# Kernel tuning notes

Measured on AMD Instinct MI355X. Metric: run time of the kernel, lower is better.

Reference implementation:

```python
import jax, jax.numpy as jnp
import numpy as np


def setup_inputs() -> dict:
    key = jax.random.key(0)
    k1, k2 = jax.random.split(key)
    B, Lq, Ls, D = 16, 2048, 2048, 512
    query = jax.random.normal(k1, (B, Lq, D), dtype=jnp.float32)
    support = jax.random.normal(k2, (B, Ls, D), dtype=jnp.float32)
    return {"query": query, "support": support}


def reference(query, support):
    # attn: [B, Lq, Ls] = softmax(query @ support^T, axis=-1)
    logits = jnp.einsum("bqd,bsd->bqs", query, support)
    attn = jax.nn.softmax(logits, axis=-1)
    # attended support: [B, Lq, D]
    attended = jnp.einsum("bqs,bsd->bqd", attn, support)
    # score: [B, Lq] = sum over D of query * attended
    score = jnp.sum(query * attended, axis=-1)
    return score
```

## Files before the change

### kernel.cpp

```cpp
#include <hip/hip_runtime.h>
#include <hip/hip_bf16.h>

#define B_  16
#define LQ  2048
#define LS  2048
#define DD  512
#define BQ  256
#define BS  256
#define BK  32
#define NSB (LS / BS)
#define NKC (DD / BK)
#define NSPLIT 2
#define T_STAGES ((NSB / NSPLIT) * NKC)

typedef short bf16x8 __attribute__((ext_vector_type(8)));
typedef float f32x4  __attribute__((ext_vector_type(4)));
typedef unsigned short u16x8 __attribute__((ext_vector_type(8)));

__device__ __forceinline__ void load_lds16(const void* g, void* l) {
  __builtin_amdgcn_global_load_lds((const __attribute__((address_space(1))) void*)g,
                                   (__attribute__((address_space(3))) void*)l,
                                   16, 0, 0);
}

__device__ __forceinline__ unsigned short f2bf(float f) {
  union { float f; unsigned int u; } v; v.f = f;
  unsigned int r = v.u + 0x7fffu + ((v.u >> 16) & 1u);
  return (unsigned short)(r >> 16);
}

__global__ __launch_bounds__(256) void cvt_kernel(const float* __restrict__ Q,
                                                  const float* __restrict__ S,
                                                  unsigned short* __restrict__ Qw,
                                                  unsigned short* __restrict__ Sw,
                                                  int nblk) {
  int blk = blockIdx.x;
  const float* src; unsigned short* dst;
  if (blk < nblk) { src = Q; dst = Qw; } else { src = S; dst = Sw; blk -= nblk; }
  int i = blk * 256 + threadIdx.x;
  float4 f0 = ((const float4*)src)[i * 2];
  float4 f1 = ((const float4*)src)[i * 2 + 1];
  u16x8 u;
  u[0] = f2bf(f0.x); u[1] = f2bf(f0.y); u[2] = f2bf(f0.z); u[3] = f2bf(f0.w);
  u[4] = f2bf(f1.x); u[5] = f2bf(f1.y); u[6] = f2bf(f1.z); u[7] = f2bf(f1.w);
  ((u16x8*)dst)[i] = u;
}

__global__ __launch_bounds__(1024, 4) void attn_kernel(const unsigned short* __restrict__ Qw,
                                                       const unsigned short* __restrict__ Sw,
                                                       float* __restrict__ pm,
                                                       float* __restrict__ pse,
                                                       float* __restrict__ psel) {
  __shared__ __align__(16) unsigned short sQ0[BQ * BK], sS0[BS * BK];
  __shared__ __align__(16) unsigned short sQ1[BQ * BK], sS1[BS * BK];
  __shared__ __align__(16) unsigned short sQ2[BQ * BK], sS2[BS * BK];
  __shared__ __align__(16) unsigned short sQ3[BQ * BK], sS3[BS * BK];

  const int id   = blockIdx.x;
  const int qb   = id >> 5;
  const int bsx  = id & 31;
  const int b    = bsx >> 1;
  const int spl  = bsx & 1;
  const int tid  = threadIdx.x;
  const int w    = tid >> 6;
  const int lane = tid & 63;
  const int h    = w & 3;
  const int g    = w >> 2;
  const int col  = lane & 15;
  const int quad = lane >> 4;

  const int q0 = qb * BQ;
  const unsigned short* Qb = Qw + (size_t)b * LQ * DD;
  const unsigned short* Sb = Sw + (size_t)b * LS * DD;

  float mst[4] = { -INFINITY, -INFINITY, -INFINITY, -INFINITY };
  float se[4]  = { 0.f, 0.f, 0.f, 0.f };
  float sel[4] = { 0.f, 0.f, 0.f, 0.f };
  f32x4 acc[4][4];

  const int qrow   = 16 * w + (lane >> 2);
  const int cchunk = (lane & 3) ^ ((lane >> 2) & 3) ^ ((lane >> 4) & 3);
  const int ldsoff = w * 512;

  const int sbs = spl * (NSB / NSPLIT);

  auto issue = [&](int t, unsigned short* bq, unsigned short* bss) {
    const int ts = t < T_STAGES ? t : T_STAGES - 1;
    const int kb = (ts & 15) * BK + cchunk * 8;
    const int s0 = (sbs + (ts >> 4)) * BS;
    load_lds16(Qb + (size_t)(q0 + qrow) * DD + kb, bq + ldsoff);
    load_lds16(Sb + (size_t)(s0 + qrow) * DD + kb, bss + ldsoff);
  };

  const int pos = (quad ^ (col & 3) ^ ((col >> 2) & 3)) * 8;

  auto compute = [&](const unsigned short* bq, const unsigned short* bss) {
    bf16x8 aq[4], asv[4];
#pragma unroll
    for (int qt = 0; qt < 4; ++qt)
      aq[qt] = *(const bf16x8*)&bq[(g * 64 + qt * 16 + col) * BK + pos];
#pragma unroll
    for (int st = 0; st < 4; ++st)
      asv[st] = *(const bf16x8*)&bss[(h * 64 + st * 16 + col) * BK + pos];
#pragma unroll
    for (int st = 0; st < 4; ++st)
#pragma unroll
      for (int qt = 0; qt < 4; ++qt)
        acc[st][qt] = __builtin_amdgcn_mfma_f32_16x16x32_bf16(asv[st], aq[qt], acc[st][qt], 0, 0, 0);
  };

  auto initacc = [&]() {
#pragma unroll
    for (int st = 0; st < 4; ++st)
#pragma unroll
      for (int qt = 0; qt < 4; ++qt)
        acc[st][qt] = (f32x4){0.f, 0.f, 0.f, 0.f};
  };

  auto epilogue = [&]() {
#pragma unroll
    for (int qt = 0; qt < 4; ++qt) {
      float lmax = mst[qt];
#pragma unroll
      for (int st = 0; st < 4; ++st)
#pragma unroll
        for (int r = 0; r < 4; ++r)
          lmax = fmaxf(lmax, acc[st][qt][r]);
      lmax = fmaxf(lmax, __shfl_xor(lmax, 16, 64));
      lmax = fmaxf(lmax, __shfl_xor(lmax, 32, 64));
      float alpha = __expf(mst[qt] - lmax);
      float pe = 0.f, pel = 0.f;
#pragma unroll
      for (int st = 0; st < 4; ++st)
#pragma unroll
        for (int r = 0; r < 4; ++r) {
          float l = acc[st][qt][r];
          float e = __expf(l - lmax);
          pe += e;
          pel = fmaf(e, l, pel);
        }
      pe  += __shfl_xor(pe, 16, 64);  pe  += __shfl_xor(pe, 32, 64);
      pel += __shfl_xor(pel, 16, 64); pel += __shfl_xor(pel, 32, 64);
      se[qt]  = fmaf(se[qt],  alpha, pe);
      sel[qt] = fmaf(sel[qt], alpha, pel);
      mst[qt] = lmax;
    }
  };

#define STEP(t, RQ, RS, WQ, WS)                                   \
  do {                                                            \
    asm volatile("s_waitcnt vmcnt(4)" ::: "memory");              \
    asm volatile("s_barrier" ::: "memory");                       \
    issue((t) + 3, WQ, WS);                                       \
    if (((t) & 15) == 0) initacc();                               \
    compute(RQ, RS);                                              \
    if (((t) & 15) == 15) epilogue();                             \
  } while (0)

  issue(0, sQ0, sS0);
  issue(1, sQ1, sS1);
  issue(2, sQ2, sS2);

  for (int tt = 0; tt < T_STAGES; tt += 4) {
    STEP(tt + 0, sQ0, sS0, sQ3, sS3);
    STEP(tt + 1, sQ1, sS1, sQ0, sS0);
    STEP(tt + 2, sQ2, sS2, sQ1, sS1);
    STEP(tt + 3, sQ3, sS3, sQ2, sS2);
  }
#undef STEP

  __syncthreads();
  float* red = (float*)&sQ0[0];
  if (quad == 0) {
#pragma unroll
    for (int qt = 0; qt < 4; ++qt) {
      int idx = ((g * 4 + h) * 4 + qt) * 16 + col;
      red[idx]        = mst[qt];
      red[1024 + idx] = se[qt];
      red[2048 + idx] = sel[qt];
    }
  }
  __syncthreads();
  if (h == 0 && quad == 0) {
#pragma unroll
    for (int qt = 0; qt < 4; ++qt) {
      float M = -INFINITY;
#pragma unroll
      for (int hh = 0; hh < 4; ++hh)
        M = fmaxf(M, red[((g * 4 + hh) * 4 + qt) * 16 + col]);
      float SE = 0.f, SEL = 0.f;
#pragma unroll
      for (int hh = 0; hh < 4; ++hh) {
        int idx = ((g * 4 + hh) * 4 + qt) * 16 + col;
        float a = __expf(red[idx] - M);
        SE  = fmaf(red[1024 + idx], a, SE);
        SEL = fmaf(red[2048 + idx], a, SEL);
      }
      size_t qi = (size_t)b * LQ + q0 + g * 64 + qt * 16 + col;
      pm[qi * NSPLIT + spl]   = M;
      pse[qi * NSPLIT + spl]  = SE;
      psel[qi * NSPLIT + spl] = SEL;
    }
  }
}

__global__ __launch_bounds__(256) void combine_kernel(const float* __restrict__ pm,
                                                      const float* __restrict__ pse,
                                                      const float* __restrict__ psel,
                                                      float* __restrict__ out) {
  int i = blockIdx.x * blockDim.x + threadIdx.x;
  if (i >= B_ * LQ) return;
  float M = -INFINITY;
#pragma unroll
  for (int s = 0; s < NSPLIT; ++s) M = fmaxf(M, pm[i * NSPLIT + s]);
  float SE = 0.f, SEL = 0.f;
#pragma unroll
  for (int s = 0; s < NSPLIT; ++s) {
    float a = __expf(pm[i * NSPLIT + s] - M);
    SE  = fmaf(pse[i * NSPLIT + s],  a, SE);
    SEL = fmaf(psel[i * NSPLIT + s], a, SEL);
  }
  out[i] = SEL / SE;
}

__global__ __launch_bounds__(256) void fallback_kernel(const float* __restrict__ Q,
                                                       const float* __restrict__ S,
                                                       float* __restrict__ out) {
  __shared__ float qv[DD];
  __shared__ float red[256];
  const int b = blockIdx.y, qi = blockIdx.x, tid = threadIdx.x;
  const float* qrow = Q + ((size_t)b * LQ + qi) * DD;
  for (int d = tid; d < DD; d += 256) qv[d] = qrow[d];
  __syncthreads();
  const float* Sb = S + (size_t)b * LS * DD;
  float m = -INFINITY, se = 0.f, sel = 0.f;
  for (int s = tid; s < LS; s += 256) {
    const float* srow = Sb + (size_t)s * DD;
    float dot = 0.f;
    for (int d = 0; d < DD; ++d) dot = fmaf(qv[d], srow[d], dot);
    float mn = fmaxf(m, dot);
    float a = __expf(m - mn);
    float e = __expf(dot - mn);
    se  = se * a + e;
    sel = sel * a + e * dot;
    m = mn;
  }
  red[tid] = m; __syncthreads();
  for (int o = 128; o > 0; o >>= 1) { if (tid < o) red[tid] = fmaxf(red[tid], red[tid + o]); __syncthreads(); }
  float M = red[0]; __syncthreads();
  float a = __expf(m - M); se *= a; sel *= a;
  red[tid] = se; __syncthreads();
  for (int o = 128; o > 0; o >>= 1) { if (tid < o) red[tid] += red[tid + o]; __syncthreads(); }
  float SE = red[0]; __syncthreads();
  red[tid] = sel; __syncthreads();
  for (int o = 128; o > 0; o >>= 1) { if (tid < o) red[tid] += red[tid + o]; __syncthreads(); }
  float SEL = red[0];
  if (tid == 0) out[(size_t)b * LQ + qi] = SEL / SE;
}

extern "C" void kernel_launch(void* const* d_in, const int* in_sizes, int n_in,
                              void* d_out, int out_size, void* d_ws, size_t ws_size,
                              hipStream_t stream) {
  const float* Q = (const float*)d_in[0];
  const float* S = (const float*)d_in[1];
  float* out = (float*)d_out;
  const size_t nelem = (size_t)B_ * LQ * DD;
  const size_t part_elems = (size_t)B_ * LQ * NSPLIT;
  const size_t need = 2 * nelem * sizeof(unsigned short)
                    + 3 * part_elems * sizeof(float);

  if (ws_size >= need) {
    unsigned short* Qw = (unsigned short*)d_ws;
    unsigned short* Sw = Qw + nelem;
    float* pm   = (float*)(Sw + nelem);
    float* pse  = pm + part_elems;
    float* psel = pse + part_elems;
    int nblk = (int)(nelem / 8 / 256);
    cvt_kernel<<<2 * nblk, 256, 0, stream>>>(Q, S, Qw, Sw, nblk);
    attn_kernel<<<(LQ / BQ) * B_ * NSPLIT, 1024, 0, stream>>>(Qw, Sw, pm, pse, psel);
    combine_kernel<<<(B_ * LQ + 255) / 256, 256, 0, stream>>>(pm, pse, psel, out);
  } else {
    fallback_kernel<<<dim3(LQ, B_), 256, 0, stream>>>(Q, S, out);
  }
}
```

Baseline: 232.6 us.

## Halve workgroup to 8 waves, each computing a 64x128 tile

Workgroups drop from 16 to 8 waves, and each wave now computes 4x8 MFMA tiles instead of 4x4. This doubles per-wave register reuse of the LDS-loaded support fragments and cuts the number of waves that synchronize at each barrier. Each thread issues two global-to-LDS loads per operand per stage, so the waitcnt threshold is raised to match. The larger accumulator set raises register pressure and may reduce occupancy. An unused leftover issue lambda with dead code remains in the source.

Result: slower. 253.5 us (+9.0%).

```diff
diff --git a/kernel.cpp b/kernel.cpp
--- a/kernel.cpp
+++ b/kernel.cpp
@@ -46,11 +46,11 @@
   ((u16x8*)dst)[i] = u;
 }
 
-__global__ __launch_bounds__(1024, 4) void attn_kernel(const unsigned short* __restrict__ Qw,
-                                                       const unsigned short* __restrict__ Sw,
-                                                       float* __restrict__ pm,
-                                                       float* __restrict__ pse,
-                                                       float* __restrict__ psel) {
+__global__ __launch_bounds__(512, 2) void attn_kernel(const unsigned short* __restrict__ Qw,
+                                                      const unsigned short* __restrict__ Sw,
+                                                      float* __restrict__ pm,
+                                                      float* __restrict__ pse,
+                                                      float* __restrict__ psel) {
   __shared__ __align__(16) unsigned short sQ0[BQ * BK], sS0[BS * BK];
   __shared__ __align__(16) unsigned short sQ1[BQ * BK], sS1[BS * BK];
   __shared__ __align__(16) unsigned short sQ2[BQ * BK], sS2[BS * BK];
@@ -73,39 +73,46 @@
   const unsigned short* Qb = Qw + (size_t)b * LQ * DD;
   const unsigned short* Sb = Sw + (size_t)b * LS * DD;
 
-  float mst[4] = { -INFINITY, -INFINITY, -INFINITY, -INFINITY };
-  float se[4]  = { 0.f, 0.f, 0.f, 0.f };
-  float sel[4] = { 0.f, 0.f, 0.f, 0.f };
-  f32x4 acc[4][4];
-
-  const int qrow   = 16 * w + (lane >> 2);
-  const int cchunk = (lane & 3) ^ ((lane >> 2) & 3) ^ ((lane >> 4) & 3);
-  const int ldsoff = w * 512;
+  float mst[8], se[8], sel[8];
+#pragma unroll
+  for (int qt = 0; qt < 8; ++qt) { mst[qt] = -INFINITY; se[qt] = 0.f; sel[qt] = 0.f; }
+  f32x4 acc[4][8];
+
+  const int rsub   = lane >> 2;
+  const int ldsoff = lane * 8;
 
   const int sbs = spl * (NSB / NSPLIT);
 
   auto issue = [&](int t, unsigned short* bq, unsigned short* bss) {
     const int ts = t < T_STAGES ? t : T_STAGES - 1;
-    const int kb = (ts & 15) * BK + cchunk * 8;
+    const int kbase = (ts & 15) * BK;
     const int s0 = (sbs + (ts >> 4)) * BS;
-    load_lds16(Qb + (size_t)(q0 + qrow) * DD + kb, bq + ldsoff);
-    load_lds16(Sb + (size_t)(s0 + qrow) * DD + kb, bss + ldsoff);
+#pragma unroll
+    for (int j = 0; j < 2; ++j) {
+      const int grp = 2 * w + j;
+      const int row = grp * 16 + rsub;
+      const int chunk = (lane & 3) ^ (rsub & 3) ^ ((rsub >> 2) & 3) ^ (grp & 3) ? 0 : 0;
+      (void)chunk;
+      const int c = ((lane & 3) ^ (row & 3) ^ ((row >> 2) & 3)) * 8;
+      load_lds16(Qb + (size_t)(q0 + row) * DD + kbase + c, bq  + grp * 512 + ldsoff - (size_t)(lane * 8) + ldsoff);
+      load_lds16(Sb + (size_t)(s0 + row) * DD + kbase + c, bss + grp * 512 + ldsoff - (size_t)(lane * 8) + ldsoff);
+    }
   };
 
   const int pos = (quad ^ (col & 3) ^ ((col >> 2) & 3)) * 8;
 
   auto compute = [&](const unsigned short* bq, const unsigned short* bss) {
-    bf16x8 aq[4], asv[4];
-#pragma unroll
-    for (int qt = 0; qt < 4; ++qt)
-      aq[qt] = *(const bf16x8*)&bq[(g * 64 + qt * 16 + col) * BK + pos];
+    bf16x8 asv[4], aq[8];
 #pragma unroll
     for (int st = 0; st < 4; ++st)
       asv[st] = *(const bf16x8*)&bss[(h * 64 + st * 16 + col) * BK + pos];
 #pragma unroll
+    for (int qt = 0; qt < 8; ++qt)
+      aq[qt] = *(const bf16x8*)&bq[(g * 128 + qt * 16 + col) * BK + pos];
+#pragma unroll
     for (int st = 0; st < 4; ++st)
 #pragma unroll
-      for (int qt = 0; qt < 4; ++qt)
+      for (int qt = 0; qt < 8; ++qt)
         acc[st][qt] = __builtin_amdgcn_mfma_f32_16x16x32_bf16(asv[st], aq[qt], acc[st][qt], 0, 0, 0);
   };
 
@@ -113,13 +120,13 @@
 #pragma unroll
     for (int st = 0; st < 4; ++st)
 #pragma unroll
-      for (int qt = 0; qt < 4; ++qt)
+      for (int qt = 0; qt < 8; ++qt)
         acc[st][qt] = (f32x4){0.f, 0.f, 0.f, 0.f};
   };
 
   auto epilogue = [&]() {
 #pragma unroll
-    for (int qt = 0; qt < 4; ++qt) {
+    for (int qt = 0; qt < 8; ++qt) {
       float lmax = mst[qt];
 #pragma unroll
       for (int st = 0; st < 4; ++st)
@@ -147,19 +154,34 @@
     }
   };
 
+#define ISSUE(t, BQp, BSp)                                                  \
+  do {                                                                      \
+    const int ts_ = (t) < T_STAGES ? (t) : T_STAGES - 1;                    \
+    const int kb_ = (ts_ & 15) * BK;                                        \
+    const int s0_ = (sbs + (ts_ >> 4)) * BS;                                \
+    _Pragma("unroll")                                                       \
+    for (int j = 0; j < 2; ++j) {                                           \
+      const int grp_ = 2 * w + j;                                           \
+      const int row_ = grp_ * 16 + rsub;                                    \
+      const int c_ = ((lane & 3) ^ (row_ & 3) ^ ((row_ >> 2) & 3)) * 8;     \
+      load_lds16(Qb + (size_t)(q0 + row_) * DD + kb_ + c_, (BQp) + grp_ * 512 + ldsoff); \
+      load_lds16(Sb + (size_t)(s0_ + row_) * DD + kb_ + c_, (BSp) + grp_ * 512 + ldsoff); \
+    }                                                                       \
+  } while (0)
+
 #define STEP(t, RQ, RS, WQ, WS)                                   \
   do {                                                            \
-    asm volatile("s_waitcnt vmcnt(4)" ::: "memory");              \
+    asm volatile("s_waitcnt vmcnt(8)" ::: "memory");              \
     asm volatile("s_barrier" ::: "memory");                       \
-    issue((t) + 3, WQ, WS);                                       \
+    ISSUE((t) + 3, WQ, WS);                                       \
     if (((t) & 15) == 0) initacc();                               \
     compute(RQ, RS);                                              \
     if (((t) & 15) == 15) epilogue();                             \
   } while (0)
 
-  issue(0, sQ0, sS0);
-  issue(1, sQ1, sS1);
-  issue(2, sQ2, sS2);
+  ISSUE(0, sQ0, sS0);
+  ISSUE(1, sQ1, sS1);
+  ISSUE(2, sQ2, sS2);
 
   for (int tt = 0; tt < T_STAGES; tt += 4) {
     STEP(tt + 0, sQ0, sS0, sQ3, sS3);
@@ -168,13 +190,14 @@
     STEP(tt + 3, sQ3, sS3, sQ2, sS2);
   }
 #undef STEP
+#undef ISSUE
 
   __syncthreads();
   float* red = (float*)&sQ0[0];
   if (quad == 0) {
 #pragma unroll
-    for (int qt = 0; qt < 4; ++qt) {
-      int idx = ((g * 4 + h) * 4 + qt) * 16 + col;
+    for (int qt = 0; qt < 8; ++qt) {
+      int idx = (((g * 4 + h) * 8) + qt) * 16 + col;
       red[idx]        = mst[qt];
       red[1024 + idx] = se[qt];
       red[2048 + idx] = sel[qt];
@@ -183,20 +206,20 @@
   __syncthreads();
   if (h == 0 && quad == 0) {
 #pragma unroll
-    for (int qt = 0; qt < 4; ++qt) {
+    for (int qt = 0; qt < 8; ++qt) {
       float M = -INFINITY;
 #pragma unroll
       for (int hh = 0; hh < 4; ++hh)
-        M = fmaxf(M, red[((g * 4 + hh) * 4 + qt) * 16 + col]);
+        M = fmaxf(M, red[(((g * 4 + hh) * 8) + qt) * 16 + col]);
       float SE = 0.f, SEL = 0.f;
 #pragma unroll
       for (int hh = 0; hh < 4; ++hh) {
-        int idx = ((g * 4 + hh) * 4 + qt) * 16 + col;
+        int idx = (((g * 4 + hh) * 8) + qt) * 16 + col;
         float a = __expf(red[idx] - M);
         SE  = fmaf(red[1024 + idx], a, SE);
         SEL = fmaf(red[2048 + idx], a, SEL);
       }
-      size_t qi = (size_t)b * LQ + q0 + g * 64 + qt * 16 + col;
+      size_t qi = (size_t)b * LQ + q0 + g * 128 + qt * 16 + col;
       pm[qi * NSPLIT + spl]   = M;
       pse[qi * NSPLIT + spl]  = SE;
       psel[qi * NSPLIT + spl] = SEL;
@@ -277,7 +300,7 @@
     float* psel = pse + part_elems;
     int nblk = (int)(nelem / 8 / 256);
     cvt_kernel<<<2 * nblk, 256, 0, stream>>>(Q, S, Qw, Sw, nblk);
-    attn_kernel<<<(LQ / BQ) * B_ * NSPLIT, 1024, 0, stream>>>(Qw, Sw, pm, pse, psel);
+    attn_kernel<<<(LQ / BQ) * B_ * NSPLIT, 512, 0, stream>>>(Qw, Sw, pm, pse, psel);
     combine_kernel<<<(B_ * LQ + 255) / 256, 256, 0, stream>>>(pm, pse, psel, out);
   } else {
     fallback_kernel<<<dim3(LQ, B_), 256, 0, stream>>>(Q, S, out);
```
